# Optimization experiments

Measured on AMD Instinct MI355X. Metric: run time of the kernel, lower is better.

## Reference

```python
import jax, jax.numpy as jnp
import numpy as np

B, T, C = 128, 256, 384
H, HD = 8, 48          # num_heads, head_dim
WINDOW = 64

def setup_inputs() -> dict:
    key = jax.random.key(0)
    ks = jax.random.split(key, 5)
    return {
        "x": jax.random.normal(ks[0], (B, T, C), dtype=jnp.float32),
        "W_qkv": jax.random.normal(ks[1], (C, 3 * C), dtype=jnp.float32) * (1.0 / np.sqrt(C)),
        "b_qkv": jax.random.normal(ks[2], (3 * C,), dtype=jnp.float32) * 0.02,
        "W_proj": jax.random.normal(ks[3], (C, C), dtype=jnp.float32) * (1.0 / np.sqrt(C)),
        "b_proj": jax.random.normal(ks[4], (C,), dtype=jnp.float32) * 0.02,
        "gate": jnp.ones((C,), dtype=jnp.float32),
    }

def reference(x, W_qkv, b_qkv, W_proj, b_proj, gate):
    Bx, Tx, Cx = x.shape
    qkv = x @ W_qkv + b_qkv                                   # [B,T,3C]
    q, k, v = jnp.split(qkv, 3, axis=-1)
    q = q.reshape(Bx, Tx, H, HD).transpose(0, 2, 1, 3)        # [B,H,T,hd]
    k = k.reshape(Bx, Tx, H, HD).transpose(0, 2, 1, 3)
    v = v.reshape(Bx, Tx, H, HD).transpose(0, 2, 1, 3)
    scale = 1.0 / np.sqrt(HD).astype(np.float32)
    att = jnp.einsum("bhqd,bhkd->bhqk", q, k) * scale        # [B,H,T,T]
    idx = jnp.arange(Tx)
    causal = idx[:, None] >= idx[None, :]                     # lower-tri
    local = jnp.abs(idx[None, :] - idx[:, None]) <= WINDOW
    mask = (causal & local)[None, None, :, :]
    att = jnp.where(mask, att, -jnp.inf)
    att = jax.nn.softmax(att, axis=-1)
    out = jnp.einsum("bhqk,bhkd->bhqd", att, v)               # [B,H,T,hd]
    out = out.transpose(0, 2, 1, 3).reshape(Bx, Tx, Cx)       # [B,T,C]
    return (out * gate) @ W_proj + b_proj
```

## Files before the change

### kernel.cpp

```cpp
#include <hip/hip_runtime.h>
#include <hip/hip_bf16.h>

typedef __attribute__((ext_vector_type(8))) short bf16x8;
typedef __attribute__((ext_vector_type(4))) float floatx4;

#define NB 128
#define NT 256
#define NC 384
#define NH 8
#define ND 48

static __device__ __forceinline__ unsigned short f2bf(float f) {
  __hip_bfloat16 h = __float2bfloat16(f);
  return __builtin_bit_cast(unsigned short, h);
}

static __device__ __forceinline__ void gload16(const unsigned short* g, unsigned short* l) {
  __builtin_amdgcn_global_load_lds(
      (const __attribute__((address_space(1))) void*)g,
      (__attribute__((address_space(3))) void*)l, 16, 0, 0);
}

__global__ __launch_bounds__(256) void k_twt(const float* __restrict__ Wq,
                                             const float* __restrict__ Wp,
                                             unsigned short* __restrict__ WqT,
                                             unsigned short* __restrict__ WpT) {
  __shared__ float T[64][65];
  int blk = blockIdx.x;
  const float* src;
  unsigned short* dst;
  int N, kt, nt;
  if (blk < 108) { src = Wq; dst = WqT; N = 1152; kt = blk / 18; nt = blk % 18; }
  else { int b2 = blk - 108; src = Wp; dst = WpT; N = 384; kt = b2 / 6; nt = b2 % 6; }
  const int k0 = kt * 64, n0 = nt * 64;
  const int t = threadIdx.x;
  const int r = t >> 2, c = (t & 3) * 16;
  const float* s = src + (size_t)(k0 + r) * N + n0 + c;
#pragma unroll
  for (int i = 0; i < 4; ++i) *(float4*)&T[r][c + i * 4] = ((const float4*)s)[i];
  __syncthreads();
  unsigned short o[16];
#pragma unroll
  for (int i = 0; i < 16; ++i) o[i] = f2bf(T[c + i][r]);
  unsigned short* dp = dst + (size_t)(n0 + r) * 384 + k0 + c;
  *(bf16x8*)dp = *(bf16x8*)&o[0];
  *(bf16x8*)(dp + 8) = *(bf16x8*)&o[8];
}

__global__ __launch_bounds__(256) void k_qkv(const float* __restrict__ x,
                                             const unsigned short* __restrict__ WqT,
                                             const float* __restrict__ bq,
                                             unsigned short* __restrict__ qkv) {
  __shared__ __align__(16) unsigned short As[2 * 128 * 32];
  __shared__ __align__(16) unsigned short Bs[2 * 128 * 32];
  const int t = threadIdx.x, lane = t & 63, w = t >> 6;
  const int wm = w >> 1, wn = w & 1;
  const int lq = lane & 15, lg = lane >> 4;
  const int m0 = blockIdx.x * 128, n0 = blockIdx.y * 128;

  const float* Ag0 = x + (size_t)(m0 + (t >> 2)) * 384 + (t & 3) * 8;
  const float* Ag1 = Ag0 + (size_t)64 * 384;
  const unsigned short* Bg = WqT + (size_t)(n0 + w * 32 + (lane >> 2)) * 384 + (lane & 3) * 8;

  floatx4 acc[4][4] = {};
  float va[16];

#define LOADA_Q(k0)                                                   \
  {                                                                   \
    *(float4*)&va[0]  = ((const float4*)(Ag0 + (k0)))[0];             \
    *(float4*)&va[4]  = ((const float4*)(Ag0 + (k0)))[1];             \
    *(float4*)&va[8]  = ((const float4*)(Ag1 + (k0)))[0];             \
    *(float4*)&va[12] = ((const float4*)(Ag1 + (k0)))[1];             \
  }
#define WRITEA_Q(buf)                                                 \
  {                                                                   \
    bf16x8 p0, p1;                                                    \
    _Pragma("unroll") for (int i = 0; i < 8; ++i) {                   \
      p0[i] = (short)f2bf(va[i]);                                     \
      p1[i] = (short)f2bf(va[8 + i]);                                 \
    }                                                                 \
    *(bf16x8*)(As + (buf)*4096 + 8 * t) = p0;                         \
    *(bf16x8*)(As + (buf)*4096 + 2048 + 8 * t) = p1;                  \
  }
#define LOADB_Q(k0, buf)                                              \
  {                                                                   \
    gload16(Bg + (k0), Bs + (buf)*4096 + (w * 32) * 32);              \
    gload16(Bg + (k0) + 16 * 384, Bs + (buf)*4096 + (w * 32 + 16) * 32); \
  }

  LOADA_Q(0);
  LOADB_Q(0, 0);
  WRITEA_Q(0);
  __syncthreads();

  int cur = 0;
  for (int k0 = 0; k0 < 384; k0 += 32) {
    const int nk = k0 + 32;
    if (nk < 384) {
      LOADA_Q(nk);
      LOADB_Q(nk, cur ^ 1);
    }
    const unsigned short* Ac = As + cur * 4096;
    const unsigned short* Bc = Bs + cur * 4096;
    bf16x8 a[4], b[4];
#pragma unroll
    for (int mt = 0; mt < 4; ++mt)
      a[mt] = *(const bf16x8*)&Ac[(wm * 64 + mt * 16 + lq) * 32 + lg * 8];
#pragma unroll
    for (int nt = 0; nt < 4; ++nt)
      b[nt] = *(const bf16x8*)&Bc[(wn * 64 + nt * 16 + lq) * 32 + lg * 8];
#pragma unroll
    for (int mt = 0; mt < 4; ++mt)
#pragma unroll
      for (int nt = 0; nt < 4; ++nt)
        acc[mt][nt] = __builtin_amdgcn_mfma_f32_16x16x32_bf16(a[mt], b[nt], acc[mt][nt], 0, 0, 0);
    if (nk < 384) WRITEA_Q(cur ^ 1);
    __syncthreads();
    cur ^= 1;
  }

  const int comp = n0 / 384;
  const int cb = n0 - comp * 384;
#pragma unroll
  for (int nt = 0; nt < 4; ++nt) {
    const int cc = cb + wn * 64 + nt * 16 + lq;
    const int h = cc / 48, d = cc - h * 48;
    const float bias = bq[n0 + wn * 64 + nt * 16 + lq];
#pragma unroll
    for (int mt = 0; mt < 4; ++mt) {
#pragma unroll
      for (int j = 0; j < 4; ++j) {
        const int row = m0 + wm * 64 + mt * 16 + lg * 4 + j;
        const int bb = row >> 8, tt = row & 255;
        qkv[((((size_t)comp * NB + bb) * NH + h) * NT + tt) * ND + d] =
            f2bf(acc[mt][nt][j] + bias);
      }
    }
  }
}

__global__ __launch_bounds__(256) void k_attn(const unsigned short* __restrict__ qkv,
                                              const float* __restrict__ gate,
                                              unsigned short* __restrict__ attg) {
  __shared__ __align__(16) unsigned short Ks[128 * 72];
  __shared__ __align__(16) unsigned short Vt[48 * 152];
  __shared__ __align__(16) unsigned short Ps[4 * 16 * 104];
  const int t = threadIdx.x;
  const int blk = blockIdx.x;
  const int tile = blk & 3;
  const int bh = blk >> 2;
  const int b = bh >> 3, h = bh & 7;
  const int base = tile * 64;
  const size_t kvoff = (size_t)bh * NT * ND;
  const unsigned short* qptr = qkv + kvoff;
  const unsigned short* kptr = qkv + (size_t)NB * NH * NT * ND + kvoff;
  const unsigned short* vptr = qkv + (size_t)2 * NB * NH * NT * ND + kvoff;

  if (t < 48) {
    bf16x8 z = {};
    *(bf16x8*)&Vt[t * 152 + 128] = z;
    *(bf16x8*)&Vt[t * 152 + 136] = z;
  }
  if (t < 128) {
    const int r = t, ka = base - 64 + r;
    unsigned short* dst = &Ks[r * 72];
    if (ka >= 0) {
      const unsigned short* src = kptr + (size_t)ka * ND;
#pragma unroll
      for (int i = 0; i < 6; ++i) *(bf16x8*)(dst + i * 8) = *(const bf16x8*)(src + i * 8);
      bf16x8 z = {};
      *(bf16x8*)(dst + 48) = z;
      *(bf16x8*)(dst + 56) = z;
    } else {
      bf16x8 z = {};
#pragma unroll
      for (int i = 0; i < 8; ++i) *(bf16x8*)(dst + i * 8) = z;
    }
  } else {
    const int r = t - 128, ka = base - 64 + r;
    if (ka >= 0) {
      const unsigned short* src = vptr + (size_t)ka * ND;
      bf16x8 vv[6];
#pragma unroll
      for (int i = 0; i < 6; ++i) vv[i] = *(const bf16x8*)(src + i * 8);
#pragma unroll
      for (int i = 0; i < 6; ++i)
#pragma unroll
        for (int j = 0; j < 8; ++j)
          Vt[(i * 8 + j) * 152 + r] = (unsigned short)vv[i][j];
    } else {
#pragma unroll
      for (int d = 0; d < 48; ++d) Vt[d * 152 + r] = 0;
    }
  }
  __syncthreads();

  const int lane = t & 63, w = t >> 6;
  const int lq = lane & 15, lg = lane >> 4;
  const int qs = base + w * 16;

  const unsigned short* qrow = qptr + (size_t)(qs + lq) * ND;
  bf16x8 aq0 = *(const bf16x8*)(qrow + lg * 8);
  bf16x8 aq1 = {};
  if (lg < 2) aq1 = *(const bf16x8*)(qrow + 32 + lg * 8);

  floatx4 s[5];
#pragma unroll
  for (int kt = 0; kt < 5; ++kt) {
    const unsigned short* kr = &Ks[(w * 16 + kt * 16 + lq) * 72];
    bf16x8 kb0 = *(const bf16x8*)(kr + lg * 8);
    bf16x8 kb1 = *(const bf16x8*)(kr + 32 + lg * 8);
    floatx4 z = {};
    z = __builtin_amdgcn_mfma_f32_16x16x32_bf16(aq0, kb0, z, 0, 0, 0);
    z = __builtin_amdgcn_mfma_f32_16x16x32_bf16(aq1, kb1, z, 0, 0, 0);
    s[kt] = z;
  }

  const float scale = 0.14433756729740643f;
  floatx4 pj[5];
#pragma unroll
  for (int j = 0; j < 4; ++j) {
    const int qa = qs + lg * 4 + j;
    float mx = -1e30f;
    float sv[5];
    bool ok[5];
#pragma unroll
    for (int kt = 0; kt < 5; ++kt) {
      const int ka = base - 64 + w * 16 + kt * 16 + lq;
      sv[kt] = s[kt][j] * scale;
      ok[kt] = (ka >= 0) && (ka <= qa) && (qa - ka <= 64);
      if (ok[kt]) mx = fmaxf(mx, sv[kt]);
    }
#pragma unroll
    for (int dd = 1; dd < 16; dd <<= 1) mx = fmaxf(mx, __shfl_xor(mx, dd));
    float sum = 0.f;
#pragma unroll
    for (int kt = 0; kt < 5; ++kt) {
      float p = ok[kt] ? __expf(sv[kt] - mx) : 0.f;
      pj[kt][j] = p;
      sum += p;
    }
#pragma unroll
    for (int dd = 1; dd < 16; dd <<= 1) sum += __shfl_xor(sum, dd);
    const float inv = 1.f / sum;
#pragma unroll
    for (int kt = 0; kt < 5; ++kt) pj[kt][j] *= inv;
  }

  unsigned short* pw = &Ps[w * 16 * 104];
#pragma unroll
  for (int kt = 0; kt < 5; ++kt)
#pragma unroll
    for (int j = 0; j < 4; ++j)
      pw[(lg * 4 + j) * 104 + kt * 16 + lq] = f2bf(pj[kt][j]);
#pragma unroll
  for (int j = 0; j < 4; ++j) pw[lq * 104 + 80 + lg * 4 + j] = 0;

  floatx4 o[3] = {};
#pragma unroll
  for (int c = 0; c < 3; ++c) {
    bf16x8 ap = *(const bf16x8*)&pw[lq * 104 + c * 32 + lg * 8];
#pragma unroll
    for (int nt = 0; nt < 3; ++nt) {
      bf16x8 av = *(const bf16x8*)&Vt[(nt * 16 + lq) * 152 + w * 16 + c * 32 + lg * 8];
      o[nt] = __builtin_amdgcn_mfma_f32_16x16x32_bf16(ap, av, o[nt], 0, 0, 0);
    }
  }
#pragma unroll
  for (int nt = 0; nt < 3; ++nt) {
    const int d = nt * 16 + lq;
    const int c = h * ND + d;
    const float g = gate[c];
#pragma unroll
    for (int j = 0; j < 4; ++j) {
      const int tt = qs + lg * 4 + j;
      attg[((size_t)b * NT + tt) * NC + c] = f2bf(o[nt][j] * g);
    }
  }
}

__global__ __launch_bounds__(256) void k_proj(const unsigned short* __restrict__ A,
                                              const unsigned short* __restrict__ WpT,
                                              const float* __restrict__ bp,
                                              float* __restrict__ out) {
  __shared__ __align__(16) unsigned short As[2 * 128 * 32];
  __shared__ __align__(16) unsigned short Bs[2 * 128 * 32];
  const int t = threadIdx.x, lane = t & 63, w = t >> 6;
  const int wm = w >> 1, wn = w & 1;
  const int lq = lane & 15, lg = lane >> 4;
  const int m0 = blockIdx.x * 128, n0 = blockIdx.y * 128;
  const unsigned short* Ag = A + (size_t)(m0 + w * 32 + (lane >> 2)) * 384 + (lane & 3) * 8;
  const unsigned short* Bg = WpT + (size_t)(n0 + w * 32 + (lane >> 2)) * 384 + (lane & 3) * 8;
  floatx4 acc[4][4] = {};

#define STAGE_P(k0, buf)                                                   \
  {                                                                        \
    gload16(Ag + (k0), As + (buf)*4096 + (w * 32) * 32);                   \
    gload16(Ag + (k0) + 16 * 384, As + (buf)*4096 + (w * 32 + 16) * 32);   \
    gload16(Bg + (k0), Bs + (buf)*4096 + (w * 32) * 32);                   \
    gload16(Bg + (k0) + 16 * 384, Bs + (buf)*4096 + (w * 32 + 16) * 32);   \
  }

  STAGE_P(0, 0);
  __syncthreads();

  int cur = 0;
  for (int k0 = 0; k0 < 384; k0 += 32) {
    const int nk = k0 + 32;
    if (nk < 384) STAGE_P(nk, cur ^ 1);
    const unsigned short* Ac = As + cur * 4096;
    const unsigned short* Bc = Bs + cur * 4096;
    bf16x8 a[4], b[4];
#pragma unroll
    for (int mt = 0; mt < 4; ++mt)
      a[mt] = *(const bf16x8*)&Ac[(wm * 64 + mt * 16 + lq) * 32 + lg * 8];
#pragma unroll
    for (int nt = 0; nt < 4; ++nt)
      b[nt] = *(const bf16x8*)&Bc[(wn * 64 + nt * 16 + lq) * 32 + lg * 8];
#pragma unroll
    for (int mt = 0; mt < 4; ++mt)
#pragma unroll
      for (int nt = 0; nt < 4; ++nt)
        acc[mt][nt] = __builtin_amdgcn_mfma_f32_16x16x32_bf16(a[mt], b[nt], acc[mt][nt], 0, 0, 0);
    __syncthreads();
    cur ^= 1;
  }
#pragma unroll
  for (int nt = 0; nt < 4; ++nt) {
    const int col = n0 + wn * 64 + nt * 16 + lq;
    const float bias = bp[col];
#pragma unroll
    for (int mt = 0; mt < 4; ++mt)
#pragma unroll
      for (int j = 0; j < 4; ++j) {
        const int row = m0 + wm * 64 + mt * 16 + lg * 4 + j;
        out[(size_t)row * 384 + col] = acc[mt][nt][j] + bias;
      }
  }
}

extern "C" void kernel_launch(void* const* d_in, const int* in_sizes, int n_in,
                              void* d_out, int out_size, void* d_ws, size_t ws_size,
                              hipStream_t stream) {
  const float* x    = (const float*)d_in[0];
  const float* Wq   = (const float*)d_in[1];
  const float* bq   = (const float*)d_in[2];
  const float* Wp   = (const float*)d_in[3];
  const float* bp   = (const float*)d_in[4];
  const float* gate = (const float*)d_in[5];

  const size_t nx = (size_t)NB * NT * NC;
  unsigned short* attg = (unsigned short*)d_ws;
  unsigned short* qkvp = attg + nx;
  unsigned short* WqT  = qkvp + (size_t)3 * NB * NH * NT * ND;
  unsigned short* WpT  = WqT + (size_t)384 * 1152;
  float* out = (float*)d_out;

  k_twt<<<dim3(144), 256, 0, stream>>>(Wq, Wp, WqT, WpT);
  k_qkv<<<dim3(256, 9), 256, 0, stream>>>(x, WqT, bq, qkvp);
  k_attn<<<dim3(4096), 256, 0, stream>>>(qkvp, gate, attg);
  k_proj<<<dim3(256, 3), 256, 0, stream>>>(attg, WpT, bp, out);
}
```

Measured before the change: 120.8 us.

## Fuse QKV projection with windowed attention per batch and head pair

Merges the QKV GEMM and the attention kernel into one kernel. Each block computes Q, K and V for one batch and two heads directly into LDS, then runs the windowed softmax attention from LDS, so the bf16 qkv tensor never goes to global memory. The weight-prep kernel also converts x to bf16 and reorders W_qkv per head group, so the fused GEMM can stream both operands with global_load_lds and XOR-swizzled LDS. The costs are a large LDS footprint, only 512 blocks of 512 threads, and redundant loads of x for every head pair, all of which can limit occupancy.

```diff
diff --git a/kernel.cpp b/kernel.cpp
--- a/kernel.cpp
+++ b/kernel.cpp
@@ -21,262 +21,265 @@
       (__attribute__((address_space(3))) void*)l, 16, 0, 0);
 }
 
-__global__ __launch_bounds__(256) void k_twt(const float* __restrict__ Wq,
-                                             const float* __restrict__ Wp,
-                                             unsigned short* __restrict__ WqT,
-                                             unsigned short* __restrict__ WpT) {
-  __shared__ float T[64][65];
-  int blk = blockIdx.x;
-  const float* src;
-  unsigned short* dst;
-  int N, kt, nt;
-  if (blk < 108) { src = Wq; dst = WqT; N = 1152; kt = blk / 18; nt = blk % 18; }
-  else { int b2 = blk - 108; src = Wp; dst = WpT; N = 384; kt = b2 / 6; nt = b2 % 6; }
-  const int k0 = kt * 64, n0 = nt * 64;
+__global__ __launch_bounds__(256) void k_prep(const float* __restrict__ x,
+                                              const float* __restrict__ Wq,
+                                              const float* __restrict__ Wp,
+                                              unsigned short* __restrict__ xbf,
+                                              unsigned short* __restrict__ Wq2,
+                                              unsigned short* __restrict__ WpT) {
+  const int blk = blockIdx.x;
   const int t = threadIdx.x;
-  const int r = t >> 2, c = (t & 3) * 16;
-  const float* s = src + (size_t)(k0 + r) * N + n0 + c;
-#pragma unroll
-  for (int i = 0; i < 4; ++i) *(float4*)&T[r][c + i * 4] = ((const float4*)s)[i];
-  __syncthreads();
-  unsigned short o[16];
-#pragma unroll
-  for (int i = 0; i < 16; ++i) o[i] = f2bf(T[c + i][r]);
-  unsigned short* dp = dst + (size_t)(n0 + r) * 384 + k0 + c;
-  *(bf16x8*)dp = *(bf16x8*)&o[0];
-  *(bf16x8*)(dp + 8) = *(bf16x8*)&o[8];
-}
-
-__global__ __launch_bounds__(256) void k_qkv(const float* __restrict__ x,
-                                             const unsigned short* __restrict__ WqT,
-                                             const float* __restrict__ bq,
-                                             unsigned short* __restrict__ qkv) {
-  __shared__ __align__(16) unsigned short As[2 * 128 * 32];
-  __shared__ __align__(16) unsigned short Bs[2 * 128 * 32];
+  if (blk < 144) {
+    __shared__ float T[64][65];
+    const float* src;
+    int N, kt, nt;
+    if (blk < 108) { src = Wq; N = 1152; kt = blk / 18; nt = blk % 18; }
+    else { int b2 = blk - 108; src = Wp; N = 384; kt = b2 / 6; nt = b2 % 6; }
+    const int k0 = kt * 64, n0 = nt * 64;
+    const int r = t >> 2, c = (t & 3) * 16;
+    const float* s = src + (size_t)(k0 + r) * N + n0 + c;
+#pragma unroll
+    for (int i = 0; i < 4; ++i) *(float4*)&T[r][c + i * 4] = ((const float4*)s)[i];
+    __syncthreads();
+    unsigned short o[16];
+#pragma unroll
+    for (int i = 0; i < 16; ++i) o[i] = f2bf(T[c + i][r]);
+    unsigned short* dp;
+    if (blk < 108) {
+      const int n = n0 + r;
+      const int hg = (n % 384) / 48;
+      const int comp = n / 384;
+      const int d = n % 48;
+      dp = Wq2 + (size_t)(hg * 144 + comp * 48 + d) * 384 + k0 + c;
+    } else {
+      dp = WpT + (size_t)(n0 + r) * 384 + k0 + c;
+    }
+    *(bf16x8*)dp = *(bf16x8*)&o[0];
+    *(bf16x8*)(dp + 8) = *(bf16x8*)&o[8];
+  } else {
+    const int n8 = (NB * NT * NC) / 8;
+    int idx = (blk - 144) * 256 + t;
+    const int stride = (gridDim.x - 144) * 256;
+    for (; idx < n8; idx += stride) {
+      const float* s = x + (size_t)idx * 8;
+      float v[8];
+      *(float4*)&v[0] = ((const float4*)s)[0];
+      *(float4*)&v[4] = ((const float4*)s)[1];
+      bf16x8 p;
+#pragma unroll
+      for (int i = 0; i < 8; ++i) p[i] = f2bf(v[i]);
+      *(bf16x8*)(xbf + (size_t)idx * 8) = p;
+    }
+  }
+}
+
+__global__ __launch_bounds__(512, 2) void k_qkattn(const unsigned short* __restrict__ xbf,
+                                                   const unsigned short* __restrict__ Wq2,
+                                                   const float* __restrict__ bq,
+                                                   const float* __restrict__ gate,
+                                                   unsigned short* __restrict__ attg) {
+  __shared__ __align__(16) unsigned short LDSU[25600 + 18432 + 18432 + 13440];
+  unsigned short* Astg = LDSU;
+  unsigned short* Bstg = LDSU + 16384;
+  unsigned short* Qs = LDSU + 25600;
+  unsigned short* Ks = Qs + 18432;
+  unsigned short* Vt = Ks + 18432;
+
   const int t = threadIdx.x, lane = t & 63, w = t >> 6;
-  const int wm = w >> 1, wn = w & 1;
   const int lq = lane & 15, lg = lane >> 4;
-  const int m0 = blockIdx.x * 128, n0 = blockIdx.y * 128;
-
-  const float* Ag0 = x + (size_t)(m0 + (t >> 2)) * 384 + (t & 3) * 8;
-  const float* Ag1 = Ag0 + (size_t)64 * 384;
-  const unsigned short* Bg = WqT + (size_t)(n0 + w * 32 + (lane >> 2)) * 384 + (lane & 3) * 8;
-
-  floatx4 acc[4][4] = {};
-  float va[16];
-
-#define LOADA_Q(k0)                                                   \
-  {                                                                   \
-    *(float4*)&va[0]  = ((const float4*)(Ag0 + (k0)))[0];             \
-    *(float4*)&va[4]  = ((const float4*)(Ag0 + (k0)))[1];             \
-    *(float4*)&va[8]  = ((const float4*)(Ag1 + (k0)))[0];             \
-    *(float4*)&va[12] = ((const float4*)(Ag1 + (k0)))[1];             \
-  }
-#define WRITEA_Q(buf)                                                 \
-  {                                                                   \
-    bf16x8 p0, p1;                                                    \
-    _Pragma("unroll") for (int i = 0; i < 8; ++i) {                   \
-      p0[i] = (short)f2bf(va[i]);                                     \
-      p1[i] = (short)f2bf(va[8 + i]);                                 \
-    }                                                                 \
-    *(bf16x8*)(As + (buf)*4096 + 8 * t) = p0;                         \
-    *(bf16x8*)(As + (buf)*4096 + 2048 + 8 * t) = p1;                  \
-  }
-#define LOADB_Q(k0, buf)                                              \
-  {                                                                   \
-    gload16(Bg + (k0), Bs + (buf)*4096 + (w * 32) * 32);              \
-    gload16(Bg + (k0) + 16 * 384, Bs + (buf)*4096 + (w * 32 + 16) * 32); \
-  }
-
-  LOADA_Q(0);
-  LOADB_Q(0, 0);
-  WRITEA_Q(0);
-  __syncthreads();
-
-  int cur = 0;
-  for (int k0 = 0; k0 < 384; k0 += 32) {
-    const int nk = k0 + 32;
-    if (nk < 384) {
-      LOADA_Q(nk);
-      LOADB_Q(nk, cur ^ 1);
-    }
-    const unsigned short* Ac = As + cur * 4096;
-    const unsigned short* Bc = Bs + cur * 4096;
-    bf16x8 a[4], b[4];
-#pragma unroll
-    for (int mt = 0; mt < 4; ++mt)
-      a[mt] = *(const bf16x8*)&Ac[(wm * 64 + mt * 16 + lq) * 32 + lg * 8];
-#pragma unroll
-    for (int nt = 0; nt < 4; ++nt)
-      b[nt] = *(const bf16x8*)&Bc[(wn * 64 + nt * 16 + lq) * 32 + lg * 8];
-#pragma unroll
-    for (int mt = 0; mt < 4; ++mt)
-#pragma unroll
-      for (int nt = 0; nt < 4; ++nt)
-        acc[mt][nt] = __builtin_amdgcn_mfma_f32_16x16x32_bf16(a[mt], b[nt], acc[mt][nt], 0, 0, 0);
-    if (nk < 384) WRITEA_Q(cur ^ 1);
-    __syncthreads();
-    cur ^= 1;
-  }
-
-  const int comp = n0 / 384;
-  const int cb = n0 - comp * 384;
-#pragma unroll
-  for (int nt = 0; nt < 4; ++nt) {
-    const int cc = cb + wn * 64 + nt * 16 + lq;
-    const int h = cc / 48, d = cc - h * 48;
-    const float bias = bq[n0 + wn * 64 + nt * 16 + lq];
-#pragma unroll
-    for (int mt = 0; mt < 4; ++mt) {
+  const int blk = blockIdx.x, b = blk >> 2, hp = blk & 3;
+  const unsigned short* xb = xbf + (size_t)b * NT * NC;
+  const float scale = 0.14433756729740643f;
+
+  {
+    bf16x8 z = {};
+    {
+      int row = t >> 1, c0 = 48 + (t & 1) * 8;
+      *(bf16x8*)&Qs[row * 72 + c0] = z;
+      *(bf16x8*)&Ks[row * 72 + c0] = z;
+    }
+    if (t < 144) {
+      int row = t / 3, c0 = 256 + (t % 3) * 8;
+      *(bf16x8*)&Vt[row * 280 + c0] = z;
+    }
+  }
+
+#define STAGE_F(k0, buf)                                                            \
+  {                                                                                 \
+    {                                                                               \
+      int r0 = w * 32 + (lane >> 2);                                                \
+      int r1 = r0 + 16;                                                             \
+      gload16(xb + (size_t)r0 * 384 + (k0) + 8 * ((lane & 3) ^ ((r0 >> 1) & 3)),    \
+              Astg + (buf)*8192 + w * 1024);                                        \
+      gload16(xb + (size_t)r1 * 384 + (k0) + 8 * ((lane & 3) ^ ((r1 >> 1) & 3)),    \
+              Astg + (buf)*8192 + w * 1024 + 512);                                  \
+    }                                                                               \
+    if (w < 4) {                                                                    \
+      int r0 = w * 32 + (lane >> 2);                                                \
+      int r1 = r0 + 16;                                                             \
+      gload16(Wh + (size_t)r0 * 384 + (k0) + 8 * ((lane & 3) ^ ((r0 >> 1) & 3)),    \
+              Bstg + (buf)*4608 + w * 1024);                                        \
+      gload16(Wh + (size_t)r1 * 384 + (k0) + 8 * ((lane & 3) ^ ((r1 >> 1) & 3)),    \
+              Bstg + (buf)*4608 + w * 1024 + 512);                                  \
+    } else if (w == 4) {                                                            \
+      int r0 = 128 + (lane >> 2);                                                   \
+      gload16(Wh + (size_t)r0 * 384 + (k0) + 8 * ((lane & 3) ^ ((r0 >> 1) & 3)),    \
+              Bstg + (buf)*4608 + 4096);                                            \
+    }                                                                               \
+  }
+
+  for (int h = 0; h < 2; ++h) {
+    const int hg = hp * 2 + h;
+    const unsigned short* Wh = Wq2 + (size_t)hg * 144 * 384;
+    __syncthreads();
+
+    floatx4 acc[2][9] = {};
+    STAGE_F(0, 0);
+    __syncthreads();
+    int cur = 0;
+    for (int k0 = 0; k0 < 384; k0 += 32) {
+      const int nk = k0 + 32;
+      if (nk < 384) STAGE_F(nk, cur ^ 1);
+      const unsigned short* Ac = Astg + cur * 8192;
+      const unsigned short* Bc = Bstg + cur * 4608;
+      bf16x8 afr[2], bfr[9];
+#pragma unroll
+      for (int mt = 0; mt < 2; ++mt) {
+        const int R = w * 32 + mt * 16 + lq;
+        afr[mt] = *(const bf16x8*)&Ac[R * 32 + 8 * (lg ^ ((R >> 1) & 3))];
+      }
+#pragma unroll
+      for (int nt = 0; nt < 9; ++nt) {
+        const int R = nt * 16 + lq;
+        bfr[nt] = *(const bf16x8*)&Bc[R * 32 + 8 * (lg ^ ((R >> 1) & 3))];
+      }
+#pragma unroll
+      for (int mt = 0; mt < 2; ++mt)
+#pragma unroll
+        for (int nt = 0; nt < 9; ++nt)
+          acc[mt][nt] = __builtin_amdgcn_mfma_f32_16x16x32_bf16(afr[mt], bfr[nt], acc[mt][nt], 0, 0, 0);
+      __syncthreads();
+      cur ^= 1;
+    }
+
+#pragma unroll
+    for (int nt = 0; nt < 9; ++nt) {
+      const int comp = nt / 3;
+      const int d = (nt % 3) * 16 + lq;
+      const float bias = bq[comp * 384 + hg * 48 + d];
+      if (comp == 0) {
+#pragma unroll
+        for (int mt = 0; mt < 2; ++mt)
+#pragma unroll
+          for (int j = 0; j < 4; ++j) {
+            const int row = w * 32 + mt * 16 + lg * 4 + j;
+            Qs[row * 72 + d] = f2bf((acc[mt][nt][j] + bias) * scale);
+          }
+      } else if (comp == 1) {
+#pragma unroll
+        for (int mt = 0; mt < 2; ++mt)
+#pragma unroll
+          for (int j = 0; j < 4; ++j) {
+            const int row = w * 32 + mt * 16 + lg * 4 + j;
+            Ks[row * 72 + d] = f2bf(acc[mt][nt][j] + bias);
+          }
+      } else {
+#pragma unroll
+        for (int mt = 0; mt < 2; ++mt) {
+          unsigned short pk[4];
+#pragma unroll
+          for (int j = 0; j < 4; ++j) pk[j] = f2bf(acc[mt][nt][j] + bias);
+          const int rowb = w * 32 + mt * 16 + lg * 4;
+          *(uint2*)&Vt[d * 280 + rowb] = *(const uint2*)pk;
+        }
+      }
+    }
+    __syncthreads();
+
+    unsigned short* Pw = LDSU + w * 1664;
+#pragma unroll
+    for (int s = 0; s < 2; ++s) {
+      const int qs = w * 32 + s * 16;
+      const int kstart = (qs >= 64) ? (qs - 64) : 0;
+
+      const unsigned short* qrow = &Qs[(size_t)(qs + lq) * 72];
+      bf16x8 aq0 = *(const bf16x8*)(qrow + lg * 8);
+      bf16x8 aq1 = *(const bf16x8*)(qrow + 32 + lg * 8);
+
+      floatx4 sv4[5];
+#pragma unroll
+      for (int kt = 0; kt < 5; ++kt) {
+        const int kr = kstart + kt * 16 + lq;
+        bf16x8 kb0 = *(const bf16x8*)&Ks[kr * 72 + lg * 8];
+        bf16x8 kb1 = *(const bf16x8*)&Ks[kr * 72 + 32 + lg * 8];
+        floatx4 z = {};
+        z = __builtin_amdgcn_mfma_f32_16x16x32_bf16(aq0, kb0, z, 0, 0, 0);
+        z = __builtin_amdgcn_mfma_f32_16x16x32_bf16(aq1, kb1, z, 0, 0, 0);
+        sv4[kt] = z;
+      }
+
+      floatx4 pj[5];
 #pragma unroll
       for (int j = 0; j < 4; ++j) {
-        const int row = m0 + wm * 64 + mt * 16 + lg * 4 + j;
-        const int bb = row >> 8, tt = row & 255;
-        qkv[((((size_t)comp * NB + bb) * NH + h) * NT + tt) * ND + d] =
-            f2bf(acc[mt][nt][j] + bias);
-      }
-    }
-  }
-}
-
-__global__ __launch_bounds__(256) void k_attn(const unsigned short* __restrict__ qkv,
-                                              const float* __restrict__ gate,
-                                              unsigned short* __restrict__ attg) {
-  __shared__ __align__(16) unsigned short Ks[128 * 72];
-  __shared__ __align__(16) unsigned short Vt[48 * 152];
-  __shared__ __align__(16) unsigned short Ps[4 * 16 * 104];
-  const int t = threadIdx.x;
-  const int blk = blockIdx.x;
-  const int tile = blk & 3;
-  const int bh = blk >> 2;
-  const int b = bh >> 3, h = bh & 7;
-  const int base = tile * 64;
-  const size_t kvoff = (size_t)bh * NT * ND;
-  const unsigned short* qptr = qkv + kvoff;
-  const unsigned short* kptr = qkv + (size_t)NB * NH * NT * ND + kvoff;
-  const unsigned short* vptr = qkv + (size_t)2 * NB * NH * NT * ND + kvoff;
-
-  if (t < 48) {
-    bf16x8 z = {};
-    *(bf16x8*)&Vt[t * 152 + 128] = z;
-    *(bf16x8*)&Vt[t * 152 + 136] = z;
-  }
-  if (t < 128) {
-    const int r = t, ka = base - 64 + r;
-    unsigned short* dst = &Ks[r * 72];
-    if (ka >= 0) {
-      const unsigned short* src = kptr + (size_t)ka * ND;
-#pragma unroll
-      for (int i = 0; i < 6; ++i) *(bf16x8*)(dst + i * 8) = *(const bf16x8*)(src + i * 8);
-      bf16x8 z = {};
-      *(bf16x8*)(dst + 48) = z;
-      *(bf16x8*)(dst + 56) = z;
-    } else {
-      bf16x8 z = {};
-#pragma unroll
-      for (int i = 0; i < 8; ++i) *(bf16x8*)(dst + i * 8) = z;
-    }
-  } else {
-    const int r = t - 128, ka = base - 64 + r;
-    if (ka >= 0) {
-      const unsigned short* src = vptr + (size_t)ka * ND;
-      bf16x8 vv[6];
-#pragma unroll
-      for (int i = 0; i < 6; ++i) vv[i] = *(const bf16x8*)(src + i * 8);
-#pragma unroll
-      for (int i = 0; i < 6; ++i)
-#pragma unroll
-        for (int j = 0; j < 8; ++j)
-          Vt[(i * 8 + j) * 152 + r] = (unsigned short)vv[i][j];
-    } else {
-#pragma unroll
-      for (int d = 0; d < 48; ++d) Vt[d * 152 + r] = 0;
-    }
-  }
-  __syncthreads();
-
-  const int lane = t & 63, w = t >> 6;
-  const int lq = lane & 15, lg = lane >> 4;
-  const int qs = base + w * 16;
-
-  const unsigned short* qrow = qptr + (size_t)(qs + lq) * ND;
-  bf16x8 aq0 = *(const bf16x8*)(qrow + lg * 8);
-  bf16x8 aq1 = {};
-  if (lg < 2) aq1 = *(const bf16x8*)(qrow + 32 + lg * 8);
-
-  floatx4 s[5];
-#pragma unroll
-  for (int kt = 0; kt < 5; ++kt) {
-    const unsigned short* kr = &Ks[(w * 16 + kt * 16 + lq) * 72];
-    bf16x8 kb0 = *(const bf16x8*)(kr + lg * 8);
-    bf16x8 kb1 = *(const bf16x8*)(kr + 32 + lg * 8);
-    floatx4 z = {};
-    z = __builtin_amdgcn_mfma_f32_16x16x32_bf16(aq0, kb0, z, 0, 0, 0);
-    z = __builtin_amdgcn_mfma_f32_16x16x32_bf16(aq1, kb1, z, 0, 0, 0);
-    s[kt] = z;
-  }
-
-  const float scale = 0.14433756729740643f;
-  floatx4 pj[5];
-#pragma unroll
-  for (int j = 0; j < 4; ++j) {
-    const int qa = qs + lg * 4 + j;
-    float mx = -1e30f;
-    float sv[5];
-    bool ok[5];
-#pragma unroll
-    for (int kt = 0; kt < 5; ++kt) {
-      const int ka = base - 64 + w * 16 + kt * 16 + lq;
-      sv[kt] = s[kt][j] * scale;
-      ok[kt] = (ka >= 0) && (ka <= qa) && (qa - ka <= 64);
-      if (ok[kt]) mx = fmaxf(mx, sv[kt]);
-    }
-#pragma unroll
-    for (int dd = 1; dd < 16; dd <<= 1) mx = fmaxf(mx, __shfl_xor(mx, dd));
-    float sum = 0.f;
-#pragma unroll
-    for (int kt = 0; kt < 5; ++kt) {
-      float p = ok[kt] ? __expf(sv[kt] - mx) : 0.f;
-      pj[kt][j] = p;
-      sum += p;
-    }
-#pragma unroll
-    for (int dd = 1; dd < 16; dd <<= 1) sum += __shfl_xor(sum, dd);
-    const float inv = 1.f / sum;
-#pragma unroll
-    for (int kt = 0; kt < 5; ++kt) pj[kt][j] *= inv;
-  }
-
-  unsigned short* pw = &Ps[w * 16 * 104];
-#pragma unroll
-  for (int kt = 0; kt < 5; ++kt)
-#pragma unroll
-    for (int j = 0; j < 4; ++j)
-      pw[(lg * 4 + j) * 104 + kt * 16 + lq] = f2bf(pj[kt][j]);
-#pragma unroll
-  for (int j = 0; j < 4; ++j) pw[lq * 104 + 80 + lg * 4 + j] = 0;
-
-  floatx4 o[3] = {};
-#pragma unroll
-  for (int c = 0; c < 3; ++c) {
-    bf16x8 ap = *(const bf16x8*)&pw[lq * 104 + c * 32 + lg * 8];
-#pragma unroll
-    for (int nt = 0; nt < 3; ++nt) {
-      bf16x8 av = *(const bf16x8*)&Vt[(nt * 16 + lq) * 152 + w * 16 + c * 32 + lg * 8];
-      o[nt] = __builtin_amdgcn_mfma_f32_16x16x32_bf16(ap, av, o[nt], 0, 0, 0);
-    }
-  }
-#pragma unroll
-  for (int nt = 0; nt < 3; ++nt) {
-    const int d = nt * 16 + lq;
-    const int c = h * ND + d;
-    const float g = gate[c];
-#pragma unroll
-    for (int j = 0; j < 4; ++j) {
-      const int tt = qs + lg * 4 + j;
-      attg[((size_t)b * NT + tt) * NC + c] = f2bf(o[nt][j] * g);
-    }
-  }
+        const int qa = qs + lg * 4 + j;
+        float mx = -1e30f;
+        float sv[5];
+        bool ok[5];
+#pragma unroll
+        for (int kt = 0; kt < 5; ++kt) {
+          const int ka = kstart + kt * 16 + lq;
+          sv[kt] = sv4[kt][j];
+          ok[kt] = (ka <= qa) && (qa - ka <= 64);
+          if (ok[kt]) mx = fmaxf(mx, sv[kt]);
+        }
+#pragma unroll
+        for (int dd = 1; dd < 16; dd <<= 1) mx = fmaxf(mx, __shfl_xor(mx, dd));
+        float sum = 0.f;
+#pragma unroll
+        for (int kt = 0; kt < 5; ++kt) {
+          float p = ok[kt] ? __expf(sv[kt] - mx) : 0.f;
+          pj[kt][j] = p;
+          sum += p;
+        }
+#pragma unroll
+        for (int dd = 1; dd < 16; dd <<= 1) sum += __shfl_xor(sum, dd);
+        const float inv = 1.f / sum;
+#pragma unroll
+        for (int kt = 0; kt < 5; ++kt) pj[kt][j] *= inv;
+      }
+
+#pragma unroll
+      for (int kt = 0; kt < 5; ++kt)
+#pragma unroll
+        for (int j = 0; j < 4; ++j)
+          Pw[(lg * 4 + j) * 104 + kt * 16 + lq] = f2bf(pj[kt][j]);
+#pragma unroll
+      for (int j = 0; j < 4; ++j) Pw[lq * 104 + 80 + lg * 4 + j] = 0;
+
+      floatx4 o[3] = {};
+#pragma unroll
+      for (int c = 0; c < 3; ++c) {
+        bf16x8 ap = *(const bf16x8*)&Pw[lq * 104 + c * 32 + lg * 8];
+#pragma unroll
+        for (int nt = 0; nt < 3; ++nt) {
+          bf16x8 av = *(const bf16x8*)&Vt[(nt * 16 + lq) * 280 + kstart + c * 32 + lg * 8];
+          o[nt] = __builtin_amdgcn_mfma_f32_16x16x32_bf16(ap, av, o[nt], 0, 0, 0);
+        }
+      }
+#pragma unroll
+      for (int nt = 0; nt < 3; ++nt) {
+        const int d = nt * 16 + lq;
+        const int cg = hg * ND + d;
+        const float g = gate[cg];
+#pragma unroll
+        for (int j = 0; j < 4; ++j) {
+          const int tt = qs + lg * 4 + j;
+          attg[((size_t)b * NT + tt) * NC + cg] = f2bf(o[nt][j] * g);
+        }
+      }
+    }
+  }
+#undef STAGE_F
 }
 
 __global__ __launch_bounds__(256) void k_proj(const unsigned short* __restrict__ A,
@@ -337,6 +340,7 @@
         out[(size_t)row * 384 + col] = acc[mt][nt][j] + bias;
       }
   }
+#undef STAGE_P
 }
 
 extern "C" void kernel_launch(void* const* d_in, const int* in_sizes, int n_in,
@@ -351,13 +355,12 @@
 
   const size_t nx = (size_t)NB * NT * NC;
   unsigned short* attg = (unsigned short*)d_ws;
-  unsigned short* qkvp = attg + nx;
-  unsigned short* WqT  = qkvp + (size_t)3 * NB * NH * NT * ND;
-  unsigned short* WpT  = WqT + (size_t)384 * 1152;
+  unsigned short* xbf  = attg + nx;
+  unsigned short* Wq2  = xbf + nx;
+  unsigned short* WpT  = Wq2 + (size_t)1152 * 384;
   float* out = (float*)d_out;
 
-  k_twt<<<dim3(144), 256, 0, stream>>>(Wq, Wp, WqT, WpT);
-  k_qkv<<<dim3(256, 9), 256, 0, stream>>>(x, WqT, bq, qkvp);
-  k_attn<<<dim3(4096), 256, 0, stream>>>(qkvp, gate, attg);
+  k_prep<<<dim3(1680), 256, 0, stream>>>(x, Wq, Wp, xbf, Wq2, WpT);
+  k_qkattn<<<dim3(512), 512, 0, stream>>>(xbf, Wq2, bq, gate, attg);
   k_proj<<<dim3(256, 3), 256, 0, stream>>>(attg, WpT, bp, out);
 }
```

New measurement: 124.4 us. 1.03x slower.
